# Kernel tuning notes

Measured on AMD Instinct MI355X. Metric: run time of the kernel, lower is better.

## Reference

```python
import jax, jax.numpy as jnp
import numpy as np

B, N, L, E = 8, 2000, 128, 2048  # batch, nodes, local_size+1, ff_hidden_dim
PENALTY = 10.0


def setup_inputs() -> dict:
    key = jax.random.key(0)
    ks = jax.random.split(key, 8)
    dist = jax.random.uniform(ks[0], (B, N, N), jnp.float32) + 1e-3  # positive distances
    theta = jax.random.normal(ks[1], (B, N, N), jnp.float32)
    ins_feature0 = jax.random.normal(ks[2], (B, N, 1), jnp.float32)
    ins_feature1 = jax.random.normal(ks[3], (B, N, 1), jnp.float32)
    d_in = 2 * L + 2
    W1 = jax.random.normal(ks[4], (d_in, E), jnp.float32) * 0.02
    b1 = jnp.zeros((E,), jnp.float32)
    W2 = jax.random.normal(ks[5], (E, L), jnp.float32) * 0.02
    b2 = jnp.zeros((L,), jnp.float32)
    return {"theta": theta, "dist": dist, "ins_feature0": ins_feature0,
            "ins_feature1": ins_feature1, "W1": W1, "b1": b1, "W2": W2, "b2": b2}


def reference(theta, dist, ins_feature0, ins_feature1, W1, b1, W2, b2):
    k = W2.shape[1]  # local_size (L)
    # smallest-k along last dim, sorted ascending (torch.topk largest=False)
    neg_vals, idx = jax.lax.top_k(-dist, k)          # [B,N,L]
    sorted_dist = -neg_vals
    sorted_dist = sorted_dist / jnp.max(sorted_dist, axis=-1, keepdims=True)
    sorted_theta = jnp.take_along_axis(theta, idx, axis=-1)  # [B,N,L]
    x_in = jnp.concatenate([sorted_dist, sorted_theta, ins_feature0, ins_feature1], axis=-1)  # [B,N,2L+2]
    edge_emb = x_in @ W1 + b1                        # [B,N,E] (no nonlinearity, as in source)
    out = edge_emb @ W2 + b2 - sorted_dist           # [B,N,L]
    b_, n_, _ = dist.shape
    bi = jnp.arange(b_)[:, None, None]
    ni = jnp.arange(n_)[None, :, None]
    out_mat = jnp.full(dist.shape, PENALTY, dist.dtype).at[bi, ni, idx].set(out)
    return out_mat
```

## Files before the change

### kernel.cpp

```cpp
#include <hip/hip_runtime.h>
#include <hip/hip_bf16.h>

#define BN 8
#define NN 2000
#define LL 128
#define EE 2048
#define DIN 258
#define KPAD 264
#define NROWS (BN*NN)
#define PENALTY_V 10.0f
#define NBINS 256
#define CANDCAP 256
#define T0 0.092f
#define SPLITK 16
#define ECHUNK (EE/SPLITK)
#define RPB 4

__global__ __launch_bounds__(256) void kA1(const float* __restrict__ W1,
                                           const float* __restrict__ b1,
                                           const float* __restrict__ W2,
                                           float* __restrict__ part) {
    __shared__ float As2[8][64];
    const int t = threadIdx.x;
    const int j = t & 127;
    const int half = t >> 7;
    const int rg = blockIdx.x >> 4;
    const int ks = blockIdx.x & 15;
    const int k0 = rg * 8;
    const int ebase = ks * ECHUNK;
    float acc[4] = {0.f, 0.f, 0.f, 0.f};
    for (int ec = ebase; ec < ebase + ECHUNK; ec += 64) {
        #pragma unroll
        for (int q = 0; q < 2; ++q) {
            int linear = q * 256 + t;
            int r8 = linear >> 6;
            int e  = linear & 63;
            int k  = k0 + r8;
            float v;
            if (k < DIN)       v = W1[k * EE + ec + e];
            else if (k == DIN) v = b1[ec + e];
            else               v = 0.0f;
            As2[r8][e] = v;
        }
        __syncthreads();
        #pragma unroll 8
        for (int e = 0; e < 64; ++e) {
            float w = W2[(ec + e) * LL + j];
            #pragma unroll
            for (int rr = 0; rr < 4; ++rr)
                acc[rr] += As2[half * 4 + rr][e] * w;
        }
        __syncthreads();
    }
    #pragma unroll
    for (int rr = 0; rr < 4; ++rr) {
        int k = k0 + half * 4 + rr;
        part[(size_t)ks * (KPAD * LL) + k * LL + j] = acc[rr];
    }
}

__global__ __launch_bounds__(256) void kA2(const float* __restrict__ part,
                                           const float* __restrict__ b2,
                                           float* __restrict__ Wc,
                                           float* __restrict__ bc) {
    const int i = blockIdx.x * 256 + threadIdx.x;
    float s = 0.f;
    #pragma unroll
    for (int q = 0; q < SPLITK; ++q) s += part[(size_t)q * (KPAD * LL) + i];
    const int k = i >> 7;
    const int j = i & 127;
    if (k == DIN)      { bc[j] = s + b2[j]; Wc[i] = 0.f; }
    else if (k > DIN)  { Wc[i] = 0.f; }
    else               { Wc[i] = s; }
}

__global__ __launch_bounds__(256) void kB(const float* __restrict__ dist,
                                          const float* __restrict__ theta,
                                          const float* __restrict__ f0,
                                          const float* __restrict__ f1,
                                          float* __restrict__ xin,
                                          int*   __restrict__ gidx) {
    __shared__ __align__(16) unsigned int hist_all[RPB][NBINS];
    __shared__ __align__(16) unsigned long long cand_all[RPB][CANDCAP];
    __shared__ __align__(16) float obuf_all[RPB][2 * LL];
    __shared__ __align__(16) int   oidx_all[RPB][LL];
    __shared__ float sdm[RPB];

    const int t = threadIdx.x;
    const int lane = t & 63;
    const int w = t >> 6;
    const int row = blockIdx.x * RPB + w;

    unsigned int* hist = hist_all[w];
    unsigned long long* cand = cand_all[w];
    float* obuf = obuf_all[w];
    int* oidx = oidx_all[w];

    {
        uint4 z4 = {0u, 0u, 0u, 0u};
        *(uint4*)&hist[lane * 4] = z4;
        unsigned long long f1v = ~0ULL;
        #pragma unroll
        for (int q = 0; q < CANDCAP / 64; ++q) cand[lane + q * 64] = f1v;
    }

    unsigned int v[32];
    const int nv = (lane < 52) ? 32 : 28;
    {
        const uint4* drow4 = (const uint4*)(dist + (size_t)row * NN);
        #pragma unroll
        for (int q = 0; q < 8; ++q) {
            int qi = q * 64 + lane;
            if (qi < NN / 4) {
                uint4 a = drow4[qi];
                v[4 * q]     = a.x;
                v[4 * q + 1] = a.y;
                v[4 * q + 2] = a.z;
                v[4 * q + 3] = a.w;
            }
        }
    }

    float T = T0;
    unsigned int qm = 0u;
    #pragma unroll
    for (int k = 0; k < 32; ++k)
        if (k < nv && __uint_as_float(v[k]) <= T) qm |= (1u << k);
    int cnt = __builtin_popcount(qm);
    #pragma unroll
    for (int d = 1; d < 64; d <<= 1) cnt += __shfl_xor(cnt, d);

    if (cnt < LL || cnt > CANDCAP) {
        unsigned int lmax = 0u;
        #pragma unroll
        for (int k = 0; k < 32; ++k) if (k < nv) lmax = max(lmax, v[k]);
        #pragma unroll
        for (int d = 1; d < 64; d <<= 1) lmax = max(lmax, (unsigned int)__shfl_xor((int)lmax, d));
        float lo = 0.0f, hi = __uint_as_float(lmax);
        if (cnt < LL) lo = T; else hi = T;
        for (int it = 0; it < 32; ++it) {
            T = 0.5f * (lo + hi);
            unsigned int m = 0u;
            #pragma unroll
            for (int k = 0; k < 32; ++k)
                if (k < nv && __uint_as_float(v[k]) <= T) m |= (1u << k);
            int c = __builtin_popcount(m);
            #pragma unroll
            for (int d = 1; d < 64; d <<= 1) c += __shfl_xor(c, d);
            qm = m;
            if (c >= LL && c <= CANDCAP) break;
            if (c < LL) lo = T; else hi = T;
        }
    }
    const float scale2 = (float)(NBINS - 1) / T;

    #pragma unroll
    for (int k = 0; k < 32; ++k) {
        if ((qm >> k) & 1u) {
            float f = __uint_as_float(v[k]);
            int b = (int)(f * scale2);
            b = b > NBINS - 1 ? NBINS - 1 : b;
            atomicAdd(&hist[b], 1u);
        }
    }

    {
        uint4* h4 = (uint4*)&hist[lane * 4];
        uint4 a0 = *h4;
        unsigned int c[4] = {a0.x, a0.y, a0.z, a0.w};
        unsigned int loc[4], run = 0;
        #pragma unroll
        for (int k = 0; k < 4; ++k) { loc[k] = run; run += c[k]; }
        unsigned int inc = run;
        #pragma unroll
        for (int d = 1; d < 64; d <<= 1) {
            unsigned int o = (unsigned int)__shfl_up((int)inc, d);
            if (lane >= d) inc += o;
        }
        const unsigned int excl = inc - run;
        uint4 s0 = {excl + loc[0], excl + loc[1], excl + loc[2], excl + loc[3]};
        *h4 = s0;
    }

    #pragma unroll
    for (int k = 0; k < 32; ++k) {
        if ((qm >> k) & 1u) {
            unsigned int bits = v[k];
            float f = __uint_as_float(bits);
            int b = (int)(f * scale2);
            b = b > NBINS - 1 ? NBINS - 1 : b;
            unsigned int old = atomicAdd(&hist[b], 0x10000u);
            unsigned int slot = (old & 0xFFFFu) + (old >> 16);
            unsigned int idx = (unsigned int)((k >> 2) * 256 + lane * 4 + (k & 3));
            if (slot < (unsigned int)CANDCAP)
                cand[slot] = ((unsigned long long)bits << 32) | idx;
        }
    }

    {
        unsigned long long key_s[CANDCAP / 64];
        float th_s[CANDCAP / 64];
        #pragma unroll
        for (int s = 0; s < CANDCAP / 64; ++s) key_s[s] = cand[lane + s * 64];
        #pragma unroll
        for (int s = 0; s < CANDCAP / 64; ++s)
            if (key_s[s] != ~0ULL)
                th_s[s] = theta[(size_t)row * NN + (unsigned int)key_s[s]];
        #pragma unroll
        for (int s = 0; s < CANDCAP / 64; ++s) {
            unsigned long long key = key_s[s];
            if (key != ~0ULL) {
                unsigned int bits = (unsigned int)(key >> 32);
                unsigned int idx  = (unsigned int)key;
                float f = __uint_as_float(bits);
                int b = (int)(f * scale2);
                b = b > NBINS - 1 ? NBINS - 1 : b;
                unsigned int word = hist[b];
                unsigned int start = word & 0xFFFFu;
                unsigned int end = start + (word >> 16);
                if (end > (unsigned int)CANDCAP) end = (unsigned int)CANDCAP;
                unsigned int r = start;
                for (unsigned int j = start; j < end; ++j) r += (cand[j] < key);
                if (r < (unsigned int)LL) {
                    obuf[r] = f;
                    obuf[LL + r] = th_s[s];
                    oidx[r] = (int)idx;
                    if (r == LL - 1) sdm[w] = f;
                }
            }
        }
    }

    {
        const float rdm = 1.0f / sdm[w];
        float* xrow = xin + (size_t)row * KPAD;
        float4 o = *(float4*)&obuf[lane * 4];
        if (lane < 32) { o.x *= rdm; o.y *= rdm; o.z *= rdm; o.w *= rdm; }
        *(float4*)&xrow[lane * 4] = o;
        if (lane == 0) {
            xrow[256] = f0[row];
            xrow[257] = f1[row];
            #pragma unroll
            for (int z = DIN; z < KPAD; ++z) xrow[z] = 0.0f;
        }
        int2 g = *(int2*)&oidx[lane * 2];
        *(int2*)&gidx[(size_t)row * LL + lane * 2] = g;
    }
}

__global__ __launch_bounds__(256) void kC(const float* __restrict__ xin,
                                          const float* __restrict__ Wc,
                                          const float* __restrict__ bc,
                                          float* __restrict__ val) {
    __shared__ __align__(16) float As[8][132];
    __shared__ __align__(16) float Bs[8][128];
    const int t = threadIdx.x;
    const int tr = t >> 4, tc = t & 15;
    const int row0 = blockIdx.x * 128;
    float acc[8][8];
    #pragma unroll
    for (int i = 0; i < 8; ++i)
        #pragma unroll
        for (int j = 0; j < 8; ++j) acc[i][j] = 0.f;

    for (int kc = 0; kc < KPAD; kc += 8) {
        #pragma unroll
        for (int q = 0; q < 4; ++q) {
            int linear = q * 256 + t;
            int m = linear >> 3, k = linear & 7;
            As[k][m] = xin[(size_t)(row0 + m) * KPAD + kc + k];
        }
        #pragma unroll
        for (int q = 0; q < 4; ++q) {
            int linear = q * 256 + t;
            int k = linear >> 7, c = linear & 127;
            Bs[k][c] = Wc[(kc + k) * LL + c];
        }
        __syncthreads();
        #pragma unroll
        for (int k = 0; k < 8; ++k) {
            float a[8], b[8];
            *(float4*)&a[0] = *(const float4*)&As[k][tr * 8];
            *(float4*)&a[4] = *(const float4*)&As[k][tr * 8 + 4];
            *(float4*)&b[0] = *(const float4*)&Bs[k][tc * 8];
            *(float4*)&b[4] = *(const float4*)&Bs[k][tc * 8 + 4];
            #pragma unroll
            for (int i = 0; i < 8; ++i)
                #pragma unroll
                for (int j = 0; j < 8; ++j)
                    acc[i][j] += a[i] * b[j];
        }
        __syncthreads();
    }
    #pragma unroll
    for (int i = 0; i < 8; ++i) {
        int r = row0 + tr * 8 + i;
        #pragma unroll
        for (int j = 0; j < 8; ++j) {
            int c = tc * 8 + j;
            val[(size_t)r * LL + c] = acc[i][j] + bc[c] - xin[(size_t)r * KPAD + c];
        }
    }
}

__global__ __launch_bounds__(256) void kD(const int* __restrict__ gidx,
                                          const float* __restrict__ val,
                                          float* __restrict__ out) {
    __shared__ __align__(16) float rowbuf[NN];
    const int t = threadIdx.x;
    const int row = blockIdx.x;
    for (int i = t; i < NN; i += 256) rowbuf[i] = PENALTY_V;
    __syncthreads();
    if (t < 128) rowbuf[gidx[(size_t)row * LL + t]] = val[(size_t)row * LL + t];
    __syncthreads();
    float4* out4 = (float4*)(out + (size_t)row * NN);
    const float4* rb4 = (const float4*)rowbuf;
    for (int q = t; q < NN / 4; q += 256) out4[q] = rb4[q];
}

extern "C" void kernel_launch(void* const* d_in, const int* in_sizes, int n_in,
                              void* d_out, int out_size, void* d_ws, size_t ws_size,
                              hipStream_t stream) {
    const float* theta = (const float*)d_in[0];
    const float* dist  = (const float*)d_in[1];
    const float* f0    = (const float*)d_in[2];
    const float* f1    = (const float*)d_in[3];
    const float* W1    = (const float*)d_in[4];
    const float* b1    = (const float*)d_in[5];
    const float* W2    = (const float*)d_in[6];
    const float* b2    = (const float*)d_in[7];
    float* out = (float*)d_out;

    char* ws = (char*)d_ws;
    float* Wc   = (float*)ws;
    float* bc   = (float*)(ws + 135168);
    float* xin  = (float*)(ws + 135680);
    int*   gidx = (int*)  (ws + 135680 + 16896000);
    float* val  = (float*)(ws + 135680 + 16896000 + 8192000);
    float* part = val;

    kA1<<<33 * SPLITK, 256, 0, stream>>>(W1, b1, W2, part);
    kA2<<<(KPAD * LL) / 256, 256, 0, stream>>>(part, b2, Wc, bc);
    kB<<<NROWS / RPB, 256, 0, stream>>>(dist, theta, f0, f1, xin, gidx);
    kC<<<NROWS / 128, 256, 0, stream>>>(xin, Wc, bc, val);
    kD<<<NROWS, 256, 0, stream>>>(gidx, val, out);
}
```

Before: 145.9 us.

## Fuse top-k selection, small GEMM and scatter into one kernel

Merges the selection kernel, the tiled GEMM kernel and the scatter kernel into a single kernel. Each block keeps its 4 rows' sorted features in a shared-memory arena, computes the 128 outputs per row against the combined weight matrix read from global memory, then reuses the arena as the penalty-filled output row buffer before writing it out. This removes the global round trips for xin, gidx and val and two kernel launches. In exchange the GEMM loses register tiling and shared-memory reuse of Wc: each block reads all of Wc once, which makes the matmul much less efficient.

Measured after the change: 122.5 us. 16.0% less time.

```diff
diff --git a/kernel.cpp b/kernel.cpp
--- a/kernel.cpp
+++ b/kernel.cpp
@@ -15,6 +15,7 @@
 #define SPLITK 16
 #define ECHUNK (EE/SPLITK)
 #define RPB 4
+#define AWORDS 2392
 
 __global__ __launch_bounds__(256) void kA1(const float* __restrict__ W1,
                                            const float* __restrict__ b1,
@@ -74,27 +75,24 @@
     else               { Wc[i] = s; }
 }
 
-__global__ __launch_bounds__(256) void kB(const float* __restrict__ dist,
+__global__ __launch_bounds__(256) void kF(const float* __restrict__ dist,
                                           const float* __restrict__ theta,
                                           const float* __restrict__ f0,
                                           const float* __restrict__ f1,
-                                          float* __restrict__ xin,
-                                          int*   __restrict__ gidx) {
-    __shared__ __align__(16) unsigned int hist_all[RPB][NBINS];
-    __shared__ __align__(16) unsigned long long cand_all[RPB][CANDCAP];
-    __shared__ __align__(16) float obuf_all[RPB][2 * LL];
-    __shared__ __align__(16) int   oidx_all[RPB][LL];
-    __shared__ float sdm[RPB];
-
+                                          const float* __restrict__ Wc,
+                                          const float* __restrict__ bc,
+                                          float* __restrict__ out) {
+    __shared__ __align__(16) unsigned int arena[RPB][AWORDS];
     const int t = threadIdx.x;
     const int lane = t & 63;
     const int w = t >> 6;
     const int row = blockIdx.x * RPB + w;
 
-    unsigned int* hist = hist_all[w];
-    unsigned long long* cand = cand_all[w];
-    float* obuf = obuf_all[w];
-    int* oidx = oidx_all[w];
+    unsigned int* A = arena[w];
+    unsigned int* hist = A;
+    unsigned long long* cand = (unsigned long long*)(A + 256);
+    float* xv = (float*)(A + 2000);
+    int* oidx = (int*)(A + 2264);
 
     {
         uint4 z4 = {0u, 0u, 0u, 0u};
@@ -222,100 +220,75 @@
                 unsigned int r = start;
                 for (unsigned int j = start; j < end; ++j) r += (cand[j] < key);
                 if (r < (unsigned int)LL) {
-                    obuf[r] = f;
-                    obuf[LL + r] = th_s[s];
+                    xv[r] = f;
+                    xv[LL + r] = th_s[s];
                     oidx[r] = (int)idx;
-                    if (r == LL - 1) sdm[w] = f;
                 }
             }
         }
     }
 
     {
-        const float rdm = 1.0f / sdm[w];
-        float* xrow = xin + (size_t)row * KPAD;
-        float4 o = *(float4*)&obuf[lane * 4];
-        if (lane < 32) { o.x *= rdm; o.y *= rdm; o.z *= rdm; o.w *= rdm; }
-        *(float4*)&xrow[lane * 4] = o;
+        const float rdm = 1.0f / xv[LL - 1];
+        xv[lane] *= rdm;
+        xv[lane + 64] *= rdm;
         if (lane == 0) {
-            xrow[256] = f0[row];
-            xrow[257] = f1[row];
+            xv[256] = f0[row];
+            xv[257] = f1[row];
             #pragma unroll
-            for (int z = DIN; z < KPAD; ++z) xrow[z] = 0.0f;
-        }
-        int2 g = *(int2*)&oidx[lane * 2];
-        *(int2*)&gidx[(size_t)row * LL + lane * 2] = g;
-    }
-}
-
-__global__ __launch_bounds__(256) void kC(const float* __restrict__ xin,
-                                          const float* __restrict__ Wc,
-                                          const float* __restrict__ bc,
-                                          float* __restrict__ val) {
-    __shared__ __align__(16) float As[8][132];
-    __shared__ __align__(16) float Bs[8][128];
-    const int t = threadIdx.x;
-    const int tr = t >> 4, tc = t & 15;
-    const int row0 = blockIdx.x * 128;
-    float acc[8][8];
-    #pragma unroll
-    for (int i = 0; i < 8; ++i)
-        #pragma unroll
-        for (int j = 0; j < 8; ++j) acc[i][j] = 0.f;
-
-    for (int kc = 0; kc < KPAD; kc += 8) {
-        #pragma unroll
-        for (int q = 0; q < 4; ++q) {
-            int linear = q * 256 + t;
-            int m = linear >> 3, k = linear & 7;
-            As[k][m] = xin[(size_t)(row0 + m) * KPAD + kc + k];
-        }
-        #pragma unroll
-        for (int q = 0; q < 4; ++q) {
-            int linear = q * 256 + t;
-            int k = linear >> 7, c = linear & 127;
-            Bs[k][c] = Wc[(kc + k) * LL + c];
-        }
-        __syncthreads();
-        #pragma unroll
-        for (int k = 0; k < 8; ++k) {
-            float a[8], b[8];
-            *(float4*)&a[0] = *(const float4*)&As[k][tr * 8];
-            *(float4*)&a[4] = *(const float4*)&As[k][tr * 8 + 4];
-            *(float4*)&b[0] = *(const float4*)&Bs[k][tc * 8];
-            *(float4*)&b[4] = *(const float4*)&Bs[k][tc * 8 + 4];
-            #pragma unroll
-            for (int i = 0; i < 8; ++i)
-                #pragma unroll
-                for (int j = 0; j < 8; ++j)
-                    acc[i][j] += a[i] * b[j];
-        }
-        __syncthreads();
-    }
-    #pragma unroll
-    for (int i = 0; i < 8; ++i) {
-        int r = row0 + tr * 8 + i;
-        #pragma unroll
-        for (int j = 0; j < 8; ++j) {
-            int c = tc * 8 + j;
-            val[(size_t)r * LL + c] = acc[i][j] + bc[c] - xin[(size_t)r * KPAD + c];
-        }
-    }
-}
-
-__global__ __launch_bounds__(256) void kD(const int* __restrict__ gidx,
-                                          const float* __restrict__ val,
-                                          float* __restrict__ out) {
-    __shared__ __align__(16) float rowbuf[NN];
-    const int t = threadIdx.x;
-    const int row = blockIdx.x;
-    for (int i = t; i < NN; i += 256) rowbuf[i] = PENALTY_V;
+            for (int z = DIN; z < KPAD; ++z) xv[z] = 0.0f;
+        }
+    }
+
     __syncthreads();
-    if (t < 128) rowbuf[gidx[(size_t)row * LL + t]] = val[(size_t)row * LL + t];
+
+    #pragma unroll
+    for (int r = 0; r < RPB; ++r) {
+        float* rb = (float*)arena[r];
+        for (int i = t; i < NN; i += 256) rb[i] = PENALTY_V;
+    }
+
+    const int j = t & 127;
+    const int rp = t >> 7;
+    const float* x0 = (const float*)(arena[2 * rp] + 2000);
+    const float* x1 = (const float*)(arena[2 * rp + 1] + 2000);
+    float acc0 = bc[j] - x0[j];
+    float acc1 = bc[j] - x1[j];
+    #pragma unroll 2
+    for (int k = 0; k < KPAD; k += 4) {
+        float4 xa = *(const float4*)&x0[k];
+        float4 xb = *(const float4*)&x1[k];
+        float w0 = Wc[(k + 0) * LL + j];
+        float w1 = Wc[(k + 1) * LL + j];
+        float w2 = Wc[(k + 2) * LL + j];
+        float w3 = Wc[(k + 3) * LL + j];
+        acc0 += xa.x * w0; acc1 += xb.x * w0;
+        acc0 += xa.y * w1; acc1 += xb.y * w1;
+        acc0 += xa.z * w2; acc1 += xb.z * w2;
+        acc0 += xa.w * w3; acc1 += xb.w * w3;
+    }
+
     __syncthreads();
-    float4* out4 = (float4*)(out + (size_t)row * NN);
-    const float4* rb4 = (const float4*)rowbuf;
-    for (int q = t; q < NN / 4; q += 256) out4[q] = rb4[q];
+
+    {
+        float* rb0 = (float*)arena[2 * rp];
+        float* rb1 = (float*)arena[2 * rp + 1];
+        const int* oi0 = (const int*)(arena[2 * rp] + 2264);
+        const int* oi1 = (const int*)(arena[2 * rp + 1] + 2264);
+        rb0[oi0[j]] = acc0;
+        rb1[oi1[j]] = acc1;
+    }
+
+    __syncthreads();
+
+    {
+        float4* o4 = (float4*)(out + (size_t)blockIdx.x * RPB * NN);
+        for (int i = t; i < RPB * (NN / 4); i += 256) {
+            int r = i / (NN / 4);
+            int q = i - r * (NN / 4);
+            o4[i] = ((const float4*)arena[r])[q];
+        }
+    }
 }
 
 extern "C" void kernel_launch(void* const* d_in, const int* in_sizes, int n_in,
@@ -334,14 +307,9 @@
     char* ws = (char*)d_ws;
     float* Wc   = (float*)ws;
     float* bc   = (float*)(ws + 135168);
-    float* xin  = (float*)(ws + 135680);
-    int*   gidx = (int*)  (ws + 135680 + 16896000);
-    float* val  = (float*)(ws + 135680 + 16896000 + 8192000);
-    float* part = val;
+    float* part = (float*)(ws + 135680);
 
     kA1<<<33 * SPLITK, 256, 0, stream>>>(W1, b1, W2, part);
     kA2<<<(KPAD * LL) / 256, 256, 0, stream>>>(part, b2, Wc, bc);
-    kB<<<NROWS / RPB, 256, 0, stream>>>(dist, theta, f0, f1, xin, gidx);
-    kC<<<NROWS / 128, 256, 0, stream>>>(xin, Wc, bc, val);
-    kD<<<NROWS, 256, 0, stream>>>(gidx, val, out);
+    kF<<<NROWS / RPB, 256, 0, stream>>>(dist, theta, f0, f1, Wc, bc, out);
 }
```
